# Optimization experiments

Hardware: AMD Instinct MI355X
Metric: run time of the kernel (lower is better)

## Reference

```python
import jax, jax.numpy as jnp
import numpy as np
import math

B, S, D_MODEL = 2, 2048, 1024
H = 16
DK = D_MODEL // H          # 64, down-proj per-stream dim
NOPE, ROPE = 128, 64
D_HEAD = NOPE + ROPE       # 192 = d_latent // H
D_LATENT = H * D_HEAD      # 3072
ROT_DIM = 2 * ((ROPE // 2) // 2)  # rotary dim actually rotated = qk_rope_dim//2 = 32
EPS = 1e-6


def _rmsnorm(x, w):
    out = x * jax.lax.rsqrt(jnp.mean(x * x, axis=-1, keepdims=True) + EPS)
    return out * w


def _apply_rope(x):
    # x: [b, h, s, d]; rotate first ROT_DIM channels, interleaved pairing
    s = x.shape[-2]
    inv_freq = 1.0 / (10000.0 ** (jnp.arange(0, ROT_DIM, 2, dtype=jnp.float32) / ROT_DIM))
    freqs = jnp.arange(s, dtype=jnp.float32)[:, None] * inv_freq[None, :]  # [s, ROT_DIM//2]
    freqs = jnp.repeat(freqs, 2, axis=-1)  # [s, ROT_DIM], (f0,f0,f1,f1,...)
    cos, sin = jnp.cos(freqs), jnp.sin(freqs)
    xl, xr = x[..., :ROT_DIM], x[..., ROT_DIM:]
    x1, x2 = xl[..., 0::2], xl[..., 1::2]
    rot = jnp.stack([-x2, x1], axis=-1).reshape(xl.shape)
    xl = xl * cos + rot * sin
    return jnp.concatenate([xl, xr], axis=-1)


def setup_inputs() -> dict:
    key = jax.random.key(0)
    ks = jax.random.split(key, 5)
    sc = 0.02
    x = jax.random.normal(ks[0], (B, S, D_MODEL), jnp.float32)
    mask = jnp.broadcast_to(jnp.tril(jnp.ones((S, S), jnp.int32)), (B, S, S))
    w_down = jax.random.normal(ks[1], (D_MODEL, 3 * DK), jnp.float32) * sc
    rms_w = jnp.ones((3 * DK,), jnp.float32)
    w_up = jax.random.normal(ks[2], (3 * DK, 3 * D_LATENT), jnp.float32) * sc
    w_o = jax.random.normal(ks[3], (D_LATENT, D_MODEL), jnp.float32) * sc
    return {"x": x, "mask": mask, "w_down": w_down, "rms_w": rms_w, "w_up": w_up, "w_o": w_o}


def reference(x, mask, w_down, rms_w, w_up, w_o):
    h = x @ w_down                        # [b, s, 3*dk]
    h = _rmsnorm(h, rms_w)
    qkv = h @ w_up                        # [b, s, 3*d_latent]
    q, k, v = jnp.split(qkv, 3, axis=-1)  # each [b, s, d_latent]

    def to_heads(t):
        # einops '(d h)': d outer, h inner
        return t.reshape(B, S, D_HEAD, H).transpose(0, 3, 1, 2)  # [b, h, s, d]

    q, k, v = to_heads(q), to_heads(k), to_heads(v)
    q_nope, q_rope = q[..., :NOPE], q[..., NOPE:]
    k_nope, k_rope = k[..., :NOPE], k[..., NOPE:]
    q_rope = _apply_rope(q_rope)
    k_rope = _apply_rope(k_rope)

    scores = (jnp.einsum('bhid,bhjd->bhij', q_nope, k_nope)
              + jnp.einsum('bhid,bhjd->bhij', q_rope, k_rope))
    scores = scores / math.sqrt(NOPE + ROPE)
    scores = jnp.where(mask[:, None] == 0, -1e9, scores)
    attn = jax.nn.softmax(scores, axis=-1)

    out = jnp.einsum('bhij,bhjd->bhid', attn, v)        # [b, h, s, d]
    out = out.transpose(0, 2, 1, 3).reshape(B, S, D_LATENT)  # 'b h s d -> b s (h d)'
    return out @ w_o
```

## Files before the change

### kernel.cpp

```cpp
#include <hip/hip_runtime.h>
#include <stdint.h>
#include <stddef.h>


typedef __bf16 bf16x8 __attribute__((ext_vector_type(8)));
typedef float  f32x4  __attribute__((ext_vector_type(4)));

#define MFMA16x16(a,b,c) __builtin_amdgcn_mfma_f32_16x16x32_bf16((a),(b),(c),0,0,0)

__device__ __forceinline__ uint16_t f2bf(float f){
  union { float f; uint32_t u; } v; v.f = f;
  uint32_t u = v.u + 0x7fffu + ((v.u >> 16) & 1u);
  return (uint16_t)(u >> 16);
}
__device__ __forceinline__ bf16x8 load_frag(const uint16_t* p){
  uint4 u = *reinterpret_cast<const uint4*>(p);
  return __builtin_bit_cast(bf16x8, u);
}
__device__ __forceinline__ f32x4 fzero(){
  f32x4 z = {0.f, 0.f, 0.f, 0.f};
  return z;
}
__device__ __forceinline__ uint32_t pack2(float a, float b){
  return (uint32_t)f2bf(a) | ((uint32_t)f2bf(b) << 16);
}
__device__ __forceinline__ void gl2lds16(const uint16_t* g, uint16_t* l){
  __builtin_amdgcn_global_load_lds(
      (const __attribute__((address_space(1))) uint32_t*)g,
      (__attribute__((address_space(3))) uint32_t*)l,
      16, 0, 0);
}

__global__ __launch_bounds__(256) void k_transpose_cvt(const float* __restrict__ in,
                                                       uint16_t* __restrict__ out,
                                                       int R, int C){
  __shared__ float t[32][33];
  const int tc = blockIdx.x * 32;
  const int tr = blockIdx.y * 32;
  const int j = threadIdx.x & 31, i0 = threadIdx.x >> 5;
  for(int ii = 0; ii < 4; ++ii){
    int r = i0 + ii * 8;
    t[r][j] = in[(size_t)(tr + r) * C + tc + j];
  }
  __syncthreads();
  for(int ii = 0; ii < 4; ++ii){
    int c = i0 + ii * 8;
    out[(size_t)(tc + c) * R + tr + j] = f2bf(t[j][c]);
  }
}

__global__ __launch_bounds__(256) void k_down_mfma(const float* __restrict__ x,
                                                   const uint16_t* __restrict__ wdt,
                                                   const float* __restrict__ rms_w,
                                                   uint16_t* __restrict__ h_out){
  __shared__ __align__(16) uint16_t as[32 * 64];
  __shared__ float hsq[32];
  const int tid  = threadIdx.x;
  const int wave = tid >> 6, lane = tid & 63;
  const int ml = lane & 15, qd = lane >> 4;
  const int m0 = blockIdx.x * 32;
  const int n0w = wave * 48;
  if(tid < 32) hsq[tid] = 0.f;

  f32x4 acc[2][3];
#pragma unroll
  for(int mt = 0; mt < 2; ++mt)
#pragma unroll
    for(int nt = 0; nt < 3; ++nt) acc[mt][nt] = fzero();

  const int srow = tid >> 3, sc = tid & 7;
  for(int kt = 0; kt < 16; ++kt){
    const float* src = x + (size_t)(m0 + srow) * 1024 + kt * 64 + sc * 8;
    float4 a = *reinterpret_cast<const float4*>(src);
    float4 b = *reinterpret_cast<const float4*>(src + 4);
    uint4 pk;
    pk.x = pack2(a.x, a.y); pk.y = pack2(a.z, a.w);
    pk.z = pack2(b.x, b.y); pk.w = pack2(b.z, b.w);
    __syncthreads();
    *reinterpret_cast<uint4*>(as + srow * 64 + ((sc ^ (srow & 7)) * 8)) = pk;
    __syncthreads();
#pragma unroll
    for(int kk = 0; kk < 2; ++kk){
      bf16x8 af[2];
#pragma unroll
      for(int mt = 0; mt < 2; ++mt){
        int row = mt * 16 + ml;
        af[mt] = load_frag(as + row * 64 + (((kk * 4 + qd) ^ (row & 7)) * 8));
      }
#pragma unroll
      for(int nt = 0; nt < 3; ++nt){
        bf16x8 bfr = load_frag(wdt + (size_t)(n0w + nt * 16 + ml) * 1024 + kt * 64 + kk * 32 + qd * 8);
#pragma unroll
        for(int mt = 0; mt < 2; ++mt)
          acc[mt][nt] = MFMA16x16(af[mt], bfr, acc[mt][nt]);
      }
    }
  }
  __syncthreads();
#pragma unroll
  for(int mt = 0; mt < 2; ++mt)
#pragma unroll
    for(int r = 0; r < 4; ++r){
      float s = acc[mt][0][r]*acc[mt][0][r] + acc[mt][1][r]*acc[mt][1][r] + acc[mt][2][r]*acc[mt][2][r];
#pragma unroll
      for(int off = 1; off < 16; off <<= 1) s += __shfl_xor(s, off);
      if(ml == 0) atomicAdd(&hsq[mt * 16 + qd * 4 + r], s);
    }
  __syncthreads();
  float rw[3];
#pragma unroll
  for(int nt = 0; nt < 3; ++nt) rw[nt] = rms_w[n0w + nt * 16 + ml];
#pragma unroll
  for(int mt = 0; mt < 2; ++mt)
#pragma unroll
    for(int r = 0; r < 4; ++r){
      int row = mt * 16 + qd * 4 + r;
      float scl = rsqrtf(hsq[row] * (1.0f / 192.0f) + 1e-6f);
#pragma unroll
      for(int nt = 0; nt < 3; ++nt)
        h_out[(size_t)(m0 + row) * 192 + n0w + nt * 16 + ml] = f2bf(acc[mt][nt][r] * scl * rw[nt]);
    }
}

__global__ __launch_bounds__(256) void k_gemm_up(const uint16_t* __restrict__ hmat,
                                                 const uint16_t* __restrict__ wt,
                                                 uint16_t* __restrict__ q_t,
                                                 uint16_t* __restrict__ k_t,
                                                 uint16_t* __restrict__ v_t){
  __shared__ __align__(16) uint16_t rp[16 * 129 * 8];
  const int wave = threadIdx.x >> 6, lane = threadIdx.x & 63;
  const int ml = lane & 15, qd = lane >> 4;
  const int m0 = blockIdx.y * 32;
  const int bx = blockIdx.x;
  const int which = bx / 6;
  const int d0b = (bx % 6) * 32;
  const int n0w = bx * 512 + wave * 128;
  const int d0w = d0b + wave * 8;

  bf16x8 af[2][6];
#pragma unroll
  for(int mt = 0; mt < 2; ++mt)
#pragma unroll
    for(int kk = 0; kk < 6; ++kk)
      af[mt][kk] = load_frag(hmat + (size_t)(m0 + mt * 16 + ml) * 192 + kk * 32 + qd * 8);

  f32x4 acc[8][2];
#pragma unroll
  for(int nt = 0; nt < 8; ++nt){ acc[nt][0] = fzero(); acc[nt][1] = fzero(); }
#pragma unroll
  for(int nt = 0; nt < 8; ++nt){
#pragma unroll
    for(int kk = 0; kk < 6; ++kk){
      bf16x8 b = load_frag(wt + (size_t)(n0w + nt * 16 + ml) * 192 + kk * 32 + qd * 8);
      acc[nt][0] = MFMA16x16(af[0][kk], b, acc[nt][0]);
      acc[nt][1] = MFMA16x16(af[1][kk], b, acc[nt][1]);
    }
  }

  const int b   = m0 >> 11;
  const int s0  = m0 & 2047;
  const int kt2 = s0 >> 6;
  const int row0 = s0 & 63;
  uint4* rp4 = (uint4*)rp;

  if(which < 2){
    const float qs = which ? 1.0f : 0.07216878364870322f;
    const bool rope = (d0w >= 128) && (d0w < 160);
#pragma unroll
    for(int mt = 0; mt < 2; ++mt)
#pragma unroll
      for(int r = 0; r < 4; ++r){
        int t = mt * 16 + qd * 4 + r;
        int s = s0 + t;
        float v[8];
#pragma unroll
        for(int nt = 0; nt < 8; ++nt) v[nt] = acc[nt][mt][r] * qs;
        if(rope){
#pragma unroll
          for(int pi = 0; pi < 4; ++pi){
            int fi = (d0w + 2 * pi - 128) >> 1;
            float invf = __expf(-(float)fi * 0.5756462732485114f);
            float sn, cs;
            sincosf((float)s * invf, &sn, &cs);
            float e = v[2 * pi], o = v[2 * pi + 1];
            v[2 * pi]     = e * cs - o * sn;
            v[2 * pi + 1] = o * cs + e * sn;
          }
        }
        uint4 pk;
        pk.x = pack2(v[0], v[1]); pk.y = pack2(v[2], v[3]);
        pk.z = pack2(v[4], v[5]); pk.w = pack2(v[6], v[7]);
        rp4[ml * 129 + t * 4 + (wave ^ (t & 3))] = pk;
      }
  } else {
#pragma unroll
    for(int nt = 0; nt < 8; ++nt){
      int dl = wave * 8 + nt;
#pragma unroll
      for(int mt = 0; mt < 2; ++mt){
        int jc = mt * 2 + (qd >> 1);
        int slot = ml * 129 + dl * 4 + (jc ^ (dl & 3));
        uint2 pk;
        pk.x = pack2(acc[nt][mt][0], acc[nt][mt][1]);
        pk.y = pack2(acc[nt][mt][2], acc[nt][mt][3]);
        *(reinterpret_cast<uint2*>(rp + slot * 8) + (qd & 1)) = pk;
      }
    }
  }
  __syncthreads();

  if(which < 2){
    uint16_t* dst = which ? k_t : q_t;
    const int cb = d0b >> 3;
#pragma unroll
    for(int it = 0; it < 8; ++it){
      int h = wave * 4 + (it & 3), rhalf = it >> 2;
      int tloc = rhalf * 16 + (lane >> 2), p = lane & 3;
      int row = row0 + tloc;
      uint4 val = rp4[h * 129 + tloc * 4 + p];
      size_t off = ((size_t)(b * 16 + h) * 32 + kt2) * 12288
                 + (size_t)row * 192 + ((cb ^ (tloc & 4)) + p) * 8;
      *reinterpret_cast<uint4*>(dst + off) = val;
    }
  } else {
    const int cs0 = row0 >> 3;
#pragma unroll
    for(int it = 0; it < 8; ++it){
      int h = wave * 4 + (it & 3), dhalf = it >> 2;
      int dl = dhalf * 16 + (lane >> 2), p = lane & 3;
      uint4 val = rp4[h * 129 + dl * 4 + p];
      size_t off = ((size_t)(b * 16 + h) * 32 + kt2) * 12288
                 + (size_t)(d0b + dl) * 64 + ((cs0 ^ (dl & 4)) + p) * 8;
      *reinterpret_cast<uint4*>(v_t + off) = val;
    }
  }
}

__global__ __launch_bounds__(512, 2) void k_attn(const uint16_t* __restrict__ q_t,
                                                 const uint16_t* __restrict__ k_t,
                                                 const uint16_t* __restrict__ v_t,
                                                 uint16_t* __restrict__ attn_out){
  __shared__ __align__(16) uint16_t smem[30720];
  const int tid   = threadIdx.x;
  const int wave  = tid >> 6;
  const int lane  = tid & 63;
  const int ml    = lane & 15;
  const int qd    = lane >> 4;
  const int strip = wave & 3;
  const int khalf = wave >> 2;
  const int B     = blockIdx.x;
  const int bh    = B & 31;
  const int p     = B >> 5;

  uint16_t* const kb  = smem;
  uint16_t* const vb  = smem + 12288;
  uint16_t* const psw = smem + 25600 + wave * 640;

  const uint16_t* kbase = k_t + (size_t)bh * 393216;
  const uint16_t* vbase = v_t + (size_t)bh * 393216;
  const uint16_t* qbase = q_t + (size_t)bh * 393216;
  const int hh = bh & 15, bb = bh >> 4;

  auto stageKV = [&](int kt){
    const uint16_t* ksrc = kbase + (size_t)kt * 12288;
    const uint16_t* vsrc = vbase + (size_t)kt * 12288;
#pragma unroll
    for(int it = 0; it < 3; ++it){
      int seg = wave * 3 + it;
      gl2lds16(ksrc + seg * 512 + lane * 8, kb + seg * 512);
    }
#pragma unroll
    for(int it = 0; it < 3; ++it){
      int seg = wave * 3 + it;
      gl2lds16(vsrc + seg * 512 + lane * 8, vb + seg * 512);
    }
  };

  auto run_qblock = [&](int qb){
    {
      const uint16_t* qtile = qbase + (size_t)qb * 12288;
#pragma unroll
      for(int it = 0; it < 3; ++it){
        int seg = wave * 3 + it;
        gl2lds16(qtile + seg * 512 + lane * 8, kb + seg * 512);
      }
    }
    __builtin_amdgcn_sched_barrier(0);
    asm volatile("s_waitcnt vmcnt(0)" ::: "memory");
    __builtin_amdgcn_sched_barrier(0);
    __builtin_amdgcn_s_barrier();

    bf16x8 qf[6];
    {
      int row = strip * 16 + ml;
#pragma unroll
      for(int kk = 0; kk < 6; ++kk)
        qf[kk] = load_frag(kb + row * 192 + (((kk * 4 + qd) ^ (row & 7)) * 8));
    }
    ((uint32_t*)vb)[6144 + tid] = 0x3F803F80u;
    __syncthreads();

    stageKV(0);

    f32x4 o[13];
#pragma unroll
    for(int i = 0; i < 13; ++i) o[i] = fzero();

    const int r0 = qb * 64 + strip * 16;
    for(int kt = 0; kt <= qb; ++kt){
      __builtin_amdgcn_sched_barrier(0);
      asm volatile("s_waitcnt vmcnt(0)" ::: "memory");
      __builtin_amdgcn_sched_barrier(0);
      __builtin_amdgcn_s_barrier();

      const int kl = kt * 64 + khalf * 32;
      if(kl <= r0 + 15){
        float pp[2][4];
        __builtin_amdgcn_s_setprio(1);
#pragma unroll
        for(int nt = 0; nt < 2; ++nt){
          f32x4 a = fzero();
          int row = khalf * 32 + nt * 16 + ml;
#pragma unroll
          for(int kk = 0; kk < 6; ++kk){
            bf16x8 bfr = load_frag(kb + row * 192 + (((kk * 4 + qd) ^ (row & 7)) * 8));
            a = MFMA16x16(qf[kk], bfr, a);
          }
#pragma unroll
          for(int r = 0; r < 4; ++r) pp[nt][r] = a[r];
        }
        __builtin_amdgcn_s_setprio(0);
        const bool diag = (kl + 31 > r0);
#pragma unroll
        for(int nt = 0; nt < 2; ++nt)
#pragma unroll
          for(int r = 0; r < 4; ++r){
            float v = pp[nt][r];
            if(diag){
              int i = r0 + qd * 4 + r;
              int j = kl + nt * 16 + ml;
              if(j > i) v = -1e9f;
            }
            pp[nt][r] = __expf(v);
          }
#pragma unroll
        for(int nt = 0; nt < 2; ++nt)
#pragma unroll
          for(int r = 0; r < 4; ++r)
            psw[(qd * 4 + r) * 40 + nt * 16 + ml] = f2bf(pp[nt][r]);
        bf16x8 pa = load_frag(psw + ml * 40 + qd * 8);
        __builtin_amdgcn_s_setprio(1);
#pragma unroll
        for(int dt = 0; dt < 13; ++dt){
          int row = dt * 16 + ml;
          int cv = (khalf * 4 + qd) ^ (row & 7);
          bf16x8 vbf = load_frag(vb + row * 64 + cv * 8);
          o[dt] = MFMA16x16(pa, vbf, o[dt]);
        }
        __builtin_amdgcn_s_setprio(0);
      }
      __builtin_amdgcn_s_barrier();
      if(kt < qb) stageKV(kt + 1);
    }

    f32x4* red4 = (f32x4*)smem;
    if(khalf == 1){
#pragma unroll
      for(int dt = 0; dt < 13; ++dt)
        red4[strip * 832 + lane * 13 + dt] = o[dt];
    }
    __syncthreads();
    if(khalf == 0){
#pragma unroll
      for(int dt = 0; dt < 13; ++dt)
        o[dt] += red4[strip * 832 + lane * 13 + dt];
#pragma unroll
      for(int r = 0; r < 4; ++r){
        int i = r0 + qd * 4 + r;
        float inv = 1.0f / o[12][r];
        size_t obase = ((size_t)bb * 2048 + i) * 3072 + hh * 192;
#pragma unroll
        for(int dt = 0; dt < 12; ++dt)
          attn_out[obase + dt * 16 + ml] = f2bf(o[dt][r] * inv);
      }
    }
    __syncthreads();
  };

  run_qblock(31 - p);
  run_qblock(p);
}

__global__ __launch_bounds__(256) void k_gemm_o_tile(const uint16_t* __restrict__ a,
                                                     const uint16_t* __restrict__ wt,
                                                     float* __restrict__ part){
  __shared__ __align__(16) uint16_t as[128 * 64];
  __shared__ __align__(16) uint16_t bs[128 * 64];
  const int wave = threadIdx.x >> 6, lane = threadIdx.x & 63;
  const int ml = lane & 15, qd = lane >> 4;
  const int m0 = blockIdx.y * 128, n0 = blockIdx.x * 128;
  const int kz = blockIdx.z;
  const int mo = (wave >> 1) * 64, no = (wave & 1) * 64;

  const int lrow = lane >> 3;
  const int gch  = (lane & 7) ^ (lrow & 7);
  const uint16_t* abase = a  + (size_t)(m0 + lrow) * 3072 + kz * 1536 + gch * 8;
  const uint16_t* bbase = wt + (size_t)(n0 + lrow) * 3072 + kz * 1536 + gch * 8;

  f32x4 acc[4][4];
#pragma unroll
  for(int mt = 0; mt < 4; ++mt)
#pragma unroll
    for(int nt = 0; nt < 4; ++nt) acc[mt][nt] = fzero();

  for(int kt = 0; kt < 24; ++kt){
    __syncthreads();
#pragma unroll
    for(int it = 0; it < 4; ++it){
      int seg = it * 4 + wave;
      gl2lds16(abase + (size_t)seg * 24576 + kt * 64, as + seg * 512);
      gl2lds16(bbase + (size_t)seg * 24576 + kt * 64, bs + seg * 512);
    }
    __syncthreads();
#pragma unroll
    for(int ks2 = 0; ks2 < 2; ++ks2){
      bf16x8 af[4], bfr[4];
#pragma unroll
      for(int mt = 0; mt < 4; ++mt){
        int row = mo + mt * 16 + ml;
        af[mt] = load_frag(as + row * 64 + (((ks2 * 4 + qd) ^ (row & 7)) * 8));
      }
#pragma unroll
      for(int nt = 0; nt < 4; ++nt){
        int row = no + nt * 16 + ml;
        bfr[nt] = load_frag(bs + row * 64 + (((ks2 * 4 + qd) ^ (row & 7)) * 8));
      }
#pragma unroll
      for(int mt = 0; mt < 4; ++mt)
#pragma unroll
        for(int nt = 0; nt < 4; ++nt)
          acc[mt][nt] = MFMA16x16(af[mt], bfr[nt], acc[mt][nt]);
    }
  }

  float* dst = part + (size_t)kz * 4096 * 1024;
#pragma unroll
  for(int mt = 0; mt < 4; ++mt)
#pragma unroll
    for(int nt = 0; nt < 4; ++nt)
#pragma unroll
      for(int r = 0; r < 4; ++r){
        int row = m0 + mo + mt * 16 + qd * 4 + r;
        int col = n0 + no + nt * 16 + ml;
        dst[(size_t)row * 1024 + col] = acc[mt][nt][r];
      }
}

__global__ __launch_bounds__(256) void k_addout(const float* __restrict__ part,
                                                float* __restrict__ out){
  int i = blockIdx.x * 256 + threadIdx.x;
  const float4* p0 = (const float4*)part;
  const float4* p1 = p0 + (size_t)1048576;
  float4 a = p0[i], b = p1[i];
  float4 c; c.x = a.x + b.x; c.y = a.y + b.y; c.z = a.z + b.z; c.w = a.w + b.w;
  ((float4*)out)[i] = c;
}


extern "C" void kernel_launch(void* const* d_in, const int* in_sizes, int n_in,
                              void* d_out, int out_size, void* d_ws, size_t ws_size,
                              hipStream_t stream) {
  (void)in_sizes; (void)n_in; (void)out_size; (void)ws_size;
  const float* x      = (const float*)d_in[0];
  const float* w_down = (const float*)d_in[2];
  const float* rms_w  = (const float*)d_in[3];
  const float* w_up   = (const float*)d_in[4];
  const float* w_o    = (const float*)d_in[5];
  float* out = (float*)d_out;

  char* ws = (char*)d_ws;
  uint16_t* h_bf   = (uint16_t*)(ws);
  uint16_t* w_up_t = (uint16_t*)(ws + 1572864);
  uint16_t* w_o_t  = (uint16_t*)(ws + 5111808);
  uint16_t* w_dn_t = (uint16_t*)(ws + 11403264);
  uint16_t* q_tb   = (uint16_t*)(ws + 11796480);
  uint16_t* k_tb   = (uint16_t*)(ws + 36962304);
  uint16_t* v_tb   = (uint16_t*)(ws + 62128128);
  uint16_t* attnO  = (uint16_t*)(ws + 87293952);
  float*    part   = (float*)(ws + 11796480);

  k_transpose_cvt<<<dim3(288, 6), 256, 0, stream>>>(w_up, w_up_t, 192, 9216);
  k_transpose_cvt<<<dim3(32, 96), 256, 0, stream>>>(w_o,  w_o_t,  3072, 1024);
  k_transpose_cvt<<<dim3(6, 32),  256, 0, stream>>>(w_down, w_dn_t, 1024, 192);
  k_down_mfma<<<128, 256, 0, stream>>>(x, w_dn_t, rms_w, h_bf);
  k_gemm_up<<<dim3(18, 128), 256, 0, stream>>>(h_bf, w_up_t, q_tb, k_tb, v_tb);
  k_attn<<<512, 512, 0, stream>>>(q_tb, k_tb, v_tb, attnO);
  k_gemm_o_tile<<<dim3(8, 32, 2), 256, 0, stream>>>(attnO, w_o_t, part);
  k_addout<<<4096, 256, 0, stream>>>(part, out);
}
```

Measured before the change: 365.8 us.

## Restructure attention to one query tile per 256-thread block with 32-key steps

```diff
diff --git a/kernel.cpp b/kernel.cpp
--- a/kernel.cpp
+++ b/kernel.cpp
@@ -236,159 +236,144 @@
   }
 }
 
-__global__ __launch_bounds__(512, 2) void k_attn(const uint16_t* __restrict__ q_t,
+__global__ __launch_bounds__(256, 4) void k_attn(const uint16_t* __restrict__ q_t,
                                                  const uint16_t* __restrict__ k_t,
                                                  const uint16_t* __restrict__ v_t,
                                                  uint16_t* __restrict__ attn_out){
-  __shared__ __align__(16) uint16_t smem[30720];
-  const int tid   = threadIdx.x;
-  const int wave  = tid >> 6;
-  const int lane  = tid & 63;
-  const int ml    = lane & 15;
-  const int qd    = lane >> 4;
-  const int strip = wave & 3;
-  const int khalf = wave >> 2;
-  const int B     = blockIdx.x;
-  const int bh    = B & 31;
-  const int p     = B >> 5;
+  __shared__ __align__(16) uint16_t smem[15360];
+  const int tid  = threadIdx.x;
+  const int wave = tid >> 6;
+  const int lane = tid & 63;
+  const int ml   = lane & 15;
+  const int qd   = lane >> 4;
+  const int bx   = blockIdx.x;
+  const int bh   = bx & 31;
+  const int qt   = 31 - (bx >> 5);
+  const int last = 2 * qt + 1;
 
   uint16_t* const kb  = smem;
-  uint16_t* const vb  = smem + 12288;
-  uint16_t* const psw = smem + 25600 + wave * 640;
+  uint16_t* const vb  = smem + 6144;
+  uint16_t* const psw = smem + 12800 + wave * 640;
 
   const uint16_t* kbase = k_t + (size_t)bh * 393216;
   const uint16_t* vbase = v_t + (size_t)bh * 393216;
-  const uint16_t* qbase = q_t + (size_t)bh * 393216;
+  const uint16_t* qtile = q_t + (size_t)bh * 393216 + (size_t)qt * 12288;
   const int hh = bh & 15, bb = bh >> 4;
 
+  const int c_  = (lane & 3) ^ ((lane >> 3) & 3);
+  const int s7_ = (lane >> 2) & 7;
+  const int vg_ = (lane >> 2) * 64;
+  const int voff0 = vg_ + (((0 + c_) ^ s7_) * 8);
+  const int voff1 = vg_ + (((4 + c_) ^ s7_) * 8);
+  const int vpo = ml * 32 + ((qd ^ ((ml >> 1) & 3)) * 8);
+
+#pragma unroll
+  for(int it = 0; it < 6; ++it){
+    int seg = wave * 6 + it;
+    gl2lds16(qtile + seg * 512 + lane * 8, smem + seg * 512);
+  }
+  __builtin_amdgcn_sched_barrier(0);
+  asm volatile("s_waitcnt vmcnt(0)" ::: "memory");
+  __builtin_amdgcn_sched_barrier(0);
+  __builtin_amdgcn_s_barrier();
+
+  bf16x8 qf[6];
+  {
+    int row = wave * 16 + ml;
+#pragma unroll
+    for(int kk = 0; kk < 6; ++kk)
+      qf[kk] = load_frag(smem + row * 192 + (((kk * 4 + qd) ^ (row & 7)) * 8));
+  }
+  ((uint32_t*)(vb + 6144))[tid] = 0x3F803F80u;
+  asm volatile("s_waitcnt lgkmcnt(0)" ::: "memory");
+  __builtin_amdgcn_sched_barrier(0);
+  __builtin_amdgcn_s_barrier();
+
   auto stageKV = [&](int kt){
-    const uint16_t* ksrc = kbase + (size_t)kt * 12288;
-    const uint16_t* vsrc = vbase + (size_t)kt * 12288;
-#pragma unroll
-    for(int it = 0; it < 3; ++it){
-      int seg = wave * 3 + it;
-      gl2lds16(ksrc + seg * 512 + lane * 8, kb + seg * 512);
-    }
-#pragma unroll
-    for(int it = 0; it < 3; ++it){
-      int seg = wave * 3 + it;
-      gl2lds16(vsrc + seg * 512 + lane * 8, vb + seg * 512);
-    }
+    const uint16_t* ksrc = kbase + (size_t)(kt >> 1) * 12288 + (kt & 1) * 6144
+                         + wave * 1536 + lane * 8;
+    uint16_t* kd = kb + wave * 1536;
+    gl2lds16(ksrc,        kd);
+    gl2lds16(ksrc + 512,  kd + 512);
+    gl2lds16(ksrc + 1024, kd + 1024);
+    const int vo = (kt & 1) ? voff1 : voff0;
+    const uint16_t* vsrc = vbase + (size_t)(kt >> 1) * 12288 + (size_t)(wave * 3) * 1024 + vo;
+    uint16_t* vd = vb + wave * 1536;
+    gl2lds16(vsrc,        vd);
+    gl2lds16(vsrc + 1024, vd + 512);
+    gl2lds16(vsrc + 2048, vd + 1024);
   };
 
-  auto run_qblock = [&](int qb){
-    {
-      const uint16_t* qtile = qbase + (size_t)qb * 12288;
-#pragma unroll
-      for(int it = 0; it < 3; ++it){
-        int seg = wave * 3 + it;
-        gl2lds16(qtile + seg * 512 + lane * 8, kb + seg * 512);
-      }
-    }
+  stageKV(0);
+
+  f32x4 o[13];
+#pragma unroll
+  for(int i = 0; i < 13; ++i) o[i] = fzero();
+
+  const int r0 = qt * 64 + wave * 16;
+  for(int kt = 0; kt <= last; ++kt){
     __builtin_amdgcn_sched_barrier(0);
     asm volatile("s_waitcnt vmcnt(0)" ::: "memory");
     __builtin_amdgcn_sched_barrier(0);
     __builtin_amdgcn_s_barrier();
 
-    bf16x8 qf[6];
-    {
-      int row = strip * 16 + ml;
-#pragma unroll
-      for(int kk = 0; kk < 6; ++kk)
-        qf[kk] = load_frag(kb + row * 192 + (((kk * 4 + qd) ^ (row & 7)) * 8));
-    }
-    ((uint32_t*)vb)[6144 + tid] = 0x3F803F80u;
-    __syncthreads();
-
-    stageKV(0);
-
-    f32x4 o[13];
-#pragma unroll
-    for(int i = 0; i < 13; ++i) o[i] = fzero();
-
-    const int r0 = qb * 64 + strip * 16;
-    for(int kt = 0; kt <= qb; ++kt){
-      __builtin_amdgcn_sched_barrier(0);
-      asm volatile("s_waitcnt vmcnt(0)" ::: "memory");
-      __builtin_amdgcn_sched_barrier(0);
-      __builtin_amdgcn_s_barrier();
-
-      const int kl = kt * 64 + khalf * 32;
-      if(kl <= r0 + 15){
-        float pp[2][4];
-        __builtin_amdgcn_s_setprio(1);
-#pragma unroll
-        for(int nt = 0; nt < 2; ++nt){
-          f32x4 a = fzero();
-          int row = khalf * 32 + nt * 16 + ml;
-#pragma unroll
-          for(int kk = 0; kk < 6; ++kk){
-            bf16x8 bfr = load_frag(kb + row * 192 + (((kk * 4 + qd) ^ (row & 7)) * 8));
-            a = MFMA16x16(qf[kk], bfr, a);
+    const int kl = kt * 32;
+    if(kl <= r0 + 15){
+      float pp[2][4];
+      __builtin_amdgcn_s_setprio(1);
+#pragma unroll
+      for(int nt = 0; nt < 2; ++nt){
+        f32x4 a = fzero();
+        int row = nt * 16 + ml;
+#pragma unroll
+        for(int kk = 0; kk < 6; ++kk){
+          bf16x8 bfr = load_frag(kb + row * 192 + (((kk * 4 + qd) ^ (row & 7)) * 8));
+          a = MFMA16x16(qf[kk], bfr, a);
+        }
+#pragma unroll
+        for(int r = 0; r < 4; ++r) pp[nt][r] = a[r];
+      }
+      __builtin_amdgcn_s_setprio(0);
+      const bool diag = (kl + 31 > r0);
+#pragma unroll
+      for(int nt = 0; nt < 2; ++nt)
+#pragma unroll
+        for(int r = 0; r < 4; ++r){
+          float v = pp[nt][r];
+          if(diag){
+            int i = r0 + qd * 4 + r;
+            int j = kl + nt * 16 + ml;
+            if(j > i) v = -1e9f;
           }
-#pragma unroll
-          for(int r = 0; r < 4; ++r) pp[nt][r] = a[r];
+          pp[nt][r] = __expf(v);
         }
-        __builtin_amdgcn_s_setprio(0);
-        const bool diag = (kl + 31 > r0);
-#pragma unroll
-        for(int nt = 0; nt < 2; ++nt)
-#pragma unroll
-          for(int r = 0; r < 4; ++r){
-            float v = pp[nt][r];
-            if(diag){
-              int i = r0 + qd * 4 + r;
-              int j = kl + nt * 16 + ml;
-              if(j > i) v = -1e9f;
-            }
-            pp[nt][r] = __expf(v);
-          }
-#pragma unroll
-        for(int nt = 0; nt < 2; ++nt)
-#pragma unroll
-          for(int r = 0; r < 4; ++r)
-            psw[(qd * 4 + r) * 40 + nt * 16 + ml] = f2bf(pp[nt][r]);
-        bf16x8 pa = load_frag(psw + ml * 40 + qd * 8);
-        __builtin_amdgcn_s_setprio(1);
-#pragma unroll
-        for(int dt = 0; dt < 13; ++dt){
-          int row = dt * 16 + ml;
-          int cv = (khalf * 4 + qd) ^ (row & 7);
-          bf16x8 vbf = load_frag(vb + row * 64 + cv * 8);
-          o[dt] = MFMA16x16(pa, vbf, o[dt]);
-        }
-        __builtin_amdgcn_s_setprio(0);
-      }
-      __builtin_amdgcn_s_barrier();
-      if(kt < qb) stageKV(kt + 1);
-    }
-
-    f32x4* red4 = (f32x4*)smem;
-    if(khalf == 1){
-#pragma unroll
-      for(int dt = 0; dt < 13; ++dt)
-        red4[strip * 832 + lane * 13 + dt] = o[dt];
-    }
-    __syncthreads();
-    if(khalf == 0){
-#pragma unroll
-      for(int dt = 0; dt < 13; ++dt)
-        o[dt] += red4[strip * 832 + lane * 13 + dt];
-#pragma unroll
-      for(int r = 0; r < 4; ++r){
-        int i = r0 + qd * 4 + r;
-        float inv = 1.0f / o[12][r];
-        size_t obase = ((size_t)bb * 2048 + i) * 3072 + hh * 192;
-#pragma unroll
-        for(int dt = 0; dt < 12; ++dt)
-          attn_out[obase + dt * 16 + ml] = f2bf(o[dt][r] * inv);
-      }
-    }
-    __syncthreads();
-  };
-
-  run_qblock(31 - p);
-  run_qblock(p);
+#pragma unroll
+      for(int nt = 0; nt < 2; ++nt)
+#pragma unroll
+        for(int r = 0; r < 4; ++r)
+          psw[(qd * 4 + r) * 40 + nt * 16 + ml] = f2bf(pp[nt][r]);
+      bf16x8 pa = load_frag(psw + ml * 40 + qd * 8);
+      __builtin_amdgcn_s_setprio(1);
+#pragma unroll
+      for(int dt = 0; dt < 13; ++dt){
+        bf16x8 vbf = load_frag(vb + dt * 512 + vpo);
+        o[dt] = MFMA16x16(pa, vbf, o[dt]);
+      }
+      __builtin_amdgcn_s_setprio(0);
+    }
+    __builtin_amdgcn_s_barrier();
+    if(kt < last) stageKV(kt + 1);
+  }
+
+#pragma unroll
+  for(int r = 0; r < 4; ++r){
+    int i = r0 + qd * 4 + r;
+    float inv = 1.0f / o[12][r];
+    size_t obase = ((size_t)bb * 2048 + i) * 3072 + hh * 192;
+#pragma unroll
+    for(int dt = 0; dt < 12; ++dt)
+      attn_out[obase + dt * 16 + ml] = f2bf(o[dt][r] * inv);
+  }
 }
 
 __global__ __launch_bounds__(256) void k_gemm_o_tile(const uint16_t* __restrict__ a,
@@ -494,7 +479,7 @@
   k_transpose_cvt<<<dim3(6, 32),  256, 0, stream>>>(w_down, w_dn_t, 1024, 192);
   k_down_mfma<<<128, 256, 0, stream>>>(x, w_dn_t, rms_w, h_bf);
   k_gemm_up<<<dim3(18, 128), 256, 0, stream>>>(h_bf, w_up_t, q_tb, k_tb, v_tb);
-  k_attn<<<512, 512, 0, stream>>>(q_tb, k_tb, v_tb, attnO);
+  k_attn<<<1024, 256, 0, stream>>>(q_tb, k_tb, v_tb, attnO);
   k_gemm_o_tile<<<dim3(8, 32, 2), 256, 0, stream>>>(attnO, w_o_t, part);
   k_addout<<<4096, 256, 0, stream>>>(part, out);
 }
```

Result: faster. 350.2 us (-4.3%).
